# Performance work log

Hardware: AMD Instinct MI355X
Metric: run time of the kernel (lower is better)

The kernel has to match this reference:

```python
import jax, jax.numpy as jnp
import numpy as np

N = 50000      # nodes
E = 800000     # edges (before self loops)
DIN = 128
DOUT = 128
NEG_SLOPE = 0.2  # PyG GATConv default


def setup_inputs() -> dict:
    key = jax.random.key(0)
    k1, k2, k3, k4, k5 = jax.random.split(key, 5)
    x = jax.random.normal(k1, (N, DIN), dtype=jnp.float32)
    edge_index = jax.random.randint(k2, (2, E), 0, N, dtype=jnp.int64)
    # GATConv params (heads=1): lin weight, att_src, att_dst, bias
    W = jax.random.normal(k3, (DIN, DOUT), dtype=jnp.float32) * (1.0 / np.sqrt(DIN))
    att_src = jax.random.normal(k4, (DOUT,), dtype=jnp.float32) * 0.1
    att_dst = jax.random.normal(k5, (DOUT,), dtype=jnp.float32) * 0.1
    bias = jnp.zeros((DOUT,), dtype=jnp.float32)
    return {"x": x, "edge_index": edge_index, "W": W,
            "att_src": att_src, "att_dst": att_dst, "bias": bias}


def reference(x, edge_index, W, att_src, att_dst, bias):
    n = x.shape[0]
    # add_self_loops=True (PyG default)
    loop = jnp.arange(n, dtype=edge_index.dtype)
    src = jnp.concatenate([edge_index[0], loop])  # [E+N] message source
    dst = jnp.concatenate([edge_index[1], loop])  # [E+N] message target

    xw = x @ W                                   # [N, DOUT]
    a_src = xw @ att_src                         # [N] per-node src logit
    a_dst = xw @ att_dst                         # [N] per-node dst logit

    e = jax.nn.leaky_relu(a_src[src] + a_dst[dst], NEG_SLOPE)  # [E+N]
    # segment softmax over destination neighborhoods
    m = jax.ops.segment_max(e, dst, num_segments=n)
    ex = jnp.exp(e - m[dst])
    denom = jax.ops.segment_sum(ex, dst, num_segments=n)
    alpha = ex / denom[dst]                      # [E+N]

    # scatter-aggregate weighted neighbor features
    out = jax.ops.segment_sum(xw[src] * alpha[:, None], dst, num_segments=n)
    out = out + bias
    # outer module applies ELU
    return jax.nn.elu(out)
```

## Files before the change

### kernel.cpp

```cpp
#include <hip/hip_runtime.h>
#include <hip/hip_bf16.h>

#define NNODES 50000
#define NEDGES 800000
#define DIM    128
#define NEG_SLOPE 0.2f

#define MB     64
#define GTILES ((NNODES + MB - 1) / MB)
#define SCHUNK 2346
#define ECHUNK 342
#define FGRID  (GTILES + SCHUNK)
#define CAP    64

#define OFF_XW    0
#define OFF_ASRC  (OFF_XW   + (size_t)NNODES*DIM*2)
#define OFF_ADST  (OFF_ASRC + (size_t)NNODES*4)
#define OFF_CNT   (OFF_ADST + (size_t)NNODES*4)
#define OFF_BKT   (OFF_CNT  + (size_t)(NNODES+16)*4)

typedef __attribute__((ext_vector_type(8))) short bf16x8;
typedef __attribute__((ext_vector_type(4))) float f32x4;

__device__ __forceinline__ float lrelu(float e) {
    return e > 0.f ? e : NEG_SLOPE * e;
}
__device__ __forceinline__ short f2bf(float f) {
    unsigned int u = __float_as_uint(f);
    u += 0x7FFFu + ((u >> 16) & 1u);
    return (short)(u >> 16);
}

__global__ __launch_bounds__(256) void k_front(
    const float* __restrict__ x, const float* __restrict__ W,
    const float* __restrict__ att_src, const float* __restrict__ att_dst,
    const int* __restrict__ ei,
    unsigned short* __restrict__ xwh, float* __restrict__ a_src,
    float* __restrict__ a_dst, int* __restrict__ cnt,
    unsigned short* __restrict__ bucket)
{
    __shared__ short xs[MB * DIM];
    __shared__ short wt[DIM * DIM];
    const int t = threadIdx.x;

    if ((blockIdx.x & 3) != 0) {
        const int sid = blockIdx.x - 1 - (blockIdx.x >> 2);
        const int lo  = sid * ECHUNK;
        int hi = lo + ECHUNK; if (hi > NEDGES) hi = NEDGES;
        for (int e = lo + t; e < hi; e += 256) {
            int src = ei[e], dst = ei[NEDGES + e];
            int pos = atomicAdd(&cnt[dst], 1);
            bucket[(size_t)dst * CAP + (pos & (CAP - 1))] = (unsigned short)src;
        }
        return;
    }

    const int lane = t & 63;
    const int wv   = t >> 6;
    const int c    = lane & 15;
    const int q    = lane >> 4;
    const int base = (blockIdx.x >> 2) * MB;

#pragma unroll
    for (int it = 0; it < 4; ++it) {
        int idx = it * 256 + t;
        int row = idx >> 4, j = idx & 15;
        float4 v0 = {0,0,0,0}, v1 = {0,0,0,0};
        if (base + row < NNODES) {
            const float4* g = (const float4*)(x + (size_t)(base + row) * DIM + j * 8);
            v0 = g[0]; v1 = g[1];
        }
        bf16x8 p;
        p[0]=f2bf(v0.x); p[1]=f2bf(v0.y); p[2]=f2bf(v0.z); p[3]=f2bf(v0.w);
        p[4]=f2bf(v1.x); p[5]=f2bf(v1.y); p[6]=f2bf(v1.z); p[7]=f2bf(v1.w);
        *(bf16x8*)&xs[row * DIM + ((j ^ (row & 15)) * 8)] = p;
    }

    {
        const int n  = t >> 1;
        const int kh = (t & 1) * 64;
#pragma unroll
        for (int jc = 0; jc < 8; ++jc) {
            int kb = kh + jc * 8;
            bf16x8 p;
#pragma unroll
            for (int e = 0; e < 8; ++e)
                p[e] = f2bf(W[(size_t)(kb + e) * DIM + n]);
            int j = kb >> 3;
            *(bf16x8*)&wt[n * DIM + ((j ^ (n & 15)) * 8)] = p;
        }
    }
    __syncthreads();

    f32x4 acc[8];
#pragma unroll
    for (int tt = 0; tt < 8; ++tt) acc[tt] = (f32x4){0.f, 0.f, 0.f, 0.f};

#pragma unroll
    for (int ks = 0; ks < 4; ++ks) {
        int j = ks * 4 + q;
        bf16x8 a = *(const bf16x8*)&xs[(wv * 16 + c) * DIM + ((j ^ c) * 8)];
#pragma unroll
        for (int tt = 0; tt < 8; ++tt) {
            bf16x8 b = *(const bf16x8*)&wt[(tt * 16 + c) * DIM + ((j ^ c) * 8)];
            acc[tt] = __builtin_amdgcn_mfma_f32_16x16x32_bf16(a, b, acc[tt], 0, 0, 0);
        }
    }

    float ps[4] = {0,0,0,0}, pd[4] = {0,0,0,0};
#pragma unroll
    for (int tt = 0; tt < 8; ++tt) {
        float as = att_src[tt * 16 + c];
        float ad = att_dst[tt * 16 + c];
#pragma unroll
        for (int r = 0; r < 4; ++r) {
            ps[r] += as * acc[tt][r];
            pd[r] += ad * acc[tt][r];
        }
    }
#pragma unroll
    for (int off = 1; off < 16; off <<= 1) {
#pragma unroll
        for (int r = 0; r < 4; ++r) {
            ps[r] += __shfl_xor(ps[r], off);
            pd[r] += __shfl_xor(pd[r], off);
        }
    }
    if (c == 0) {
#pragma unroll
        for (int r = 0; r < 4; ++r) {
            int node = base + wv * 16 + q * 4 + r;
            if (node < NNODES) { a_src[node] = ps[r]; a_dst[node] = pd[r]; }
        }
    }

#pragma unroll
    for (int r = 0; r < 4; ++r) {
        int node = base + wv * 16 + q * 4 + r;
        if (node < NNODES) {
#pragma unroll
            for (int tt = 0; tt < 8; ++tt)
                xwh[(size_t)node * DIM + tt * 16 + c] = (unsigned short)f2bf(acc[tt][r]);
        }
    }
}

__global__ __launch_bounds__(256) void k_agg(
    const unsigned short* __restrict__ xwh, const float* __restrict__ a_src,
    const float* __restrict__ a_dst, const int* __restrict__ cnt,
    const unsigned short* __restrict__ bucket, const float* __restrict__ bias,
    float* __restrict__ out)
{
    const int lane = threadIdx.x & 63;
    const int n    = blockIdx.x * 4 + (threadIdx.x >> 6);

    const __hip_bfloat162* __restrict__ xw2 = (const __hip_bfloat162*)xwh;

    const int B = cnt[NNODES];
    int deg = cnt[n] - B;
    deg = deg < CAP ? deg : CAP;
    const int b0 = B & (CAP - 1);

    const float adn = a_dst[n];

    unsigned int src_l = bucket[(size_t)n * CAP + lane];
    if (src_l >= NNODES) src_l = 0;
    float w_l = __expf(lrelu(a_src[src_l] + adn));
    unsigned int u = __float_as_uint(w_l);
    u += 0x7FFFu + ((u >> 16) & 1u);
    const unsigned int entry = (u & 0xFFFF0000u) | src_l;

    float w0 = __expf(lrelu(a_src[n] + adn));
    float2 v0 = __bfloat1622float2(xw2[(size_t)n * 64 + lane]);
    float l = w0;
    float2 acc = { w0 * v0.x, w0 * v0.y };

    for (int j = 0; j < deg; j += 4) {
        float w[4];
        __hip_bfloat162 v[4];
#pragma unroll
        for (int k = 0; k < 4; ++k) {
            if (j + k < deg) {
                unsigned int e = __shfl(entry, (b0 + j + k) & (CAP - 1));
                w[k] = __uint_as_float(e & 0xFFFF0000u);
                v[k] = xw2[(size_t)(e & 0xFFFFu) * 64 + lane];
            } else {
                w[k] = 0.f;
                v[k] = xw2[lane];
            }
        }
#pragma unroll
        for (int k = 0; k < 4; ++k) {
            float2 f = __bfloat1622float2(v[k]);
            acc.x += w[k] * f.x;
            acc.y += w[k] * f.y;
            l += w[k];
        }
    }

    float2 b = ((const float2*)bias)[lane];
    float ox = acc.x / l + b.x;
    float oy = acc.y / l + b.y;
    ox = ox > 0.f ? ox : (__expf(ox) - 1.f);
    oy = oy > 0.f ? oy : (__expf(oy) - 1.f);
    float2 r = { ox, oy };
    ((float2*)out)[(size_t)n * 64 + lane] = r;
}

extern "C" void kernel_launch(void* const* d_in, const int* in_sizes, int n_in,
                              void* d_out, int out_size, void* d_ws, size_t ws_size,
                              hipStream_t stream)
{
    const float* x       = (const float*)d_in[0];
    const int*   ei      = (const int*)d_in[1];
    const float* W       = (const float*)d_in[2];
    const float* att_src = (const float*)d_in[3];
    const float* att_dst = (const float*)d_in[4];
    const float* bias    = (const float*)d_in[5];
    float*       out     = (float*)d_out;

    char* ws = (char*)d_ws;
    unsigned short* xwh = (unsigned short*)(ws + OFF_XW);
    float* a_src  = (float*)(ws + OFF_ASRC);
    float* a_dst  = (float*)(ws + OFF_ADST);
    int*   cnt    = (int*)  (ws + OFF_CNT);
    unsigned short* bucket = (unsigned short*)(ws + OFF_BKT);

    k_front<<<FGRID, 256, 0, stream>>>(x, W, att_src, att_dst, ei,
                                       xwh, a_src, a_dst, cnt, bucket);
    k_agg<<<NNODES / 4, 256, 0, stream>>>(xwh, a_src, a_dst, cnt, bucket, bias, out);
}
```

Measured before the change: 180.3 us.

## Pad degree counters, batch edge scatter, load GEMM A-fragments directly, unroll aggregation

Each degree counter now sits in its own 64-byte slot, which is meant to cut atomic contention and false sharing between neighbouring nodes. The edge-scatter blocks change to one scatter block per GEMM tile, each taking 1024 edges, and issue all loads, then all atomics, then nontemporal bucket stores. The GEMM reads its x A-fragments straight from global into registers and drops the LDS staging buffer for x. The aggregation loop is unrolled to 8 neighbours to keep more gathers in flight, and the output uses nontemporal stores. In exchange the counter array takes much more memory, and the atomics touch more distinct cache lines.

```diff
diff --git a/kernel.cpp b/kernel.cpp
--- a/kernel.cpp
+++ b/kernel.cpp
@@ -8,19 +8,20 @@
 
 #define MB     64
 #define GTILES ((NNODES + MB - 1) / MB)
-#define SCHUNK 2346
-#define ECHUNK 342
-#define FGRID  (GTILES + SCHUNK)
+#define ECHUNK 1024
+#define FGRID  (GTILES * 2)
 #define CAP    64
+#define CSTR   16
 
 #define OFF_XW    0
 #define OFF_ASRC  (OFF_XW   + (size_t)NNODES*DIM*2)
 #define OFF_ADST  (OFF_ASRC + (size_t)NNODES*4)
 #define OFF_CNT   (OFF_ADST + (size_t)NNODES*4)
-#define OFF_BKT   (OFF_CNT  + (size_t)(NNODES+16)*4)
+#define OFF_BKT   (OFF_CNT  + (size_t)(NNODES+1)*CSTR*4)
 
 typedef __attribute__((ext_vector_type(8))) short bf16x8;
 typedef __attribute__((ext_vector_type(4))) float f32x4;
+typedef __attribute__((ext_vector_type(2))) float f32x2;
 
 __device__ __forceinline__ float lrelu(float e) {
     return e > 0.f ? e : NEG_SLOPE * e;
@@ -39,19 +40,29 @@
     float* __restrict__ a_dst, int* __restrict__ cnt,
     unsigned short* __restrict__ bucket)
 {
-    __shared__ short xs[MB * DIM];
     __shared__ short wt[DIM * DIM];
     const int t = threadIdx.x;
 
-    if ((blockIdx.x & 3) != 0) {
-        const int sid = blockIdx.x - 1 - (blockIdx.x >> 2);
+    if (blockIdx.x & 1) {
+        const int sid = blockIdx.x >> 1;
         const int lo  = sid * ECHUNK;
         int hi = lo + ECHUNK; if (hi > NEDGES) hi = NEDGES;
-        for (int e = lo + t; e < hi; e += 256) {
-            int src = ei[e], dst = ei[NEDGES + e];
-            int pos = atomicAdd(&cnt[dst], 1);
-            bucket[(size_t)dst * CAP + (pos & (CAP - 1))] = (unsigned short)src;
-        }
+        int s[4], d[4], p[4];
+#pragma unroll
+        for (int k = 0; k < 4; ++k) {
+            int e = lo + t + (k << 8);
+            if (e < hi) { s[k] = ei[e]; d[k] = ei[NEDGES + e]; }
+            else d[k] = -1;
+        }
+#pragma unroll
+        for (int k = 0; k < 4; ++k)
+            if (d[k] >= 0) p[k] = atomicAdd(&cnt[(size_t)d[k] * CSTR], 1);
+#pragma unroll
+        for (int k = 0; k < 4; ++k)
+            if (d[k] >= 0)
+                __builtin_nontemporal_store(
+                    (unsigned short)s[k],
+                    &bucket[(size_t)d[k] * CAP + (p[k] & (CAP - 1))]);
         return;
     }
 
@@ -59,21 +70,20 @@
     const int wv   = t >> 6;
     const int c    = lane & 15;
     const int q    = lane >> 4;
-    const int base = (blockIdx.x >> 2) * MB;
-
-#pragma unroll
-    for (int it = 0; it < 4; ++it) {
-        int idx = it * 256 + t;
-        int row = idx >> 4, j = idx & 15;
-        float4 v0 = {0,0,0,0}, v1 = {0,0,0,0};
-        if (base + row < NNODES) {
-            const float4* g = (const float4*)(x + (size_t)(base + row) * DIM + j * 8);
-            v0 = g[0]; v1 = g[1];
-        }
-        bf16x8 p;
-        p[0]=f2bf(v0.x); p[1]=f2bf(v0.y); p[2]=f2bf(v0.z); p[3]=f2bf(v0.w);
-        p[4]=f2bf(v1.x); p[5]=f2bf(v1.y); p[6]=f2bf(v1.z); p[7]=f2bf(v1.w);
-        *(bf16x8*)&xs[row * DIM + ((j ^ (row & 15)) * 8)] = p;
+    const int base = (blockIdx.x >> 1) * MB;
+
+    int arow = base + wv * 16 + c;
+    if (arow >= NNODES) arow = 0;
+    const float4* __restrict__ xr = (const float4*)(x + (size_t)arow * DIM);
+    bf16x8 afr[4];
+#pragma unroll
+    for (int ks = 0; ks < 4; ++ks) {
+        int j = ks * 4 + q;
+        float4 v0 = xr[j * 2], v1 = xr[j * 2 + 1];
+        afr[ks][0]=f2bf(v0.x); afr[ks][1]=f2bf(v0.y);
+        afr[ks][2]=f2bf(v0.z); afr[ks][3]=f2bf(v0.w);
+        afr[ks][4]=f2bf(v1.x); afr[ks][5]=f2bf(v1.y);
+        afr[ks][6]=f2bf(v1.z); afr[ks][7]=f2bf(v1.w);
     }
 
     {
@@ -99,11 +109,10 @@
 #pragma unroll
     for (int ks = 0; ks < 4; ++ks) {
         int j = ks * 4 + q;
-        bf16x8 a = *(const bf16x8*)&xs[(wv * 16 + c) * DIM + ((j ^ c) * 8)];
 #pragma unroll
         for (int tt = 0; tt < 8; ++tt) {
             bf16x8 b = *(const bf16x8*)&wt[(tt * 16 + c) * DIM + ((j ^ c) * 8)];
-            acc[tt] = __builtin_amdgcn_mfma_f32_16x16x32_bf16(a, b, acc[tt], 0, 0, 0);
+            acc[tt] = __builtin_amdgcn_mfma_f32_16x16x32_bf16(afr[ks], b, acc[tt], 0, 0, 0);
         }
     }
 
@@ -156,8 +165,8 @@
 
     const __hip_bfloat162* __restrict__ xw2 = (const __hip_bfloat162*)xwh;
 
-    const int B = cnt[NNODES];
-    int deg = cnt[n] - B;
+    const int B = cnt[(size_t)NNODES * CSTR];
+    int deg = cnt[(size_t)n * CSTR] - B;
     deg = deg < CAP ? deg : CAP;
     const int b0 = B & (CAP - 1);
 
@@ -175,11 +184,11 @@
     float l = w0;
     float2 acc = { w0 * v0.x, w0 * v0.y };
 
-    for (int j = 0; j < deg; j += 4) {
-        float w[4];
-        __hip_bfloat162 v[4];
-#pragma unroll
-        for (int k = 0; k < 4; ++k) {
+    for (int j = 0; j < deg; j += 8) {
+        float w[8];
+        __hip_bfloat162 v[8];
+#pragma unroll
+        for (int k = 0; k < 8; ++k) {
             if (j + k < deg) {
                 unsigned int e = __shfl(entry, (b0 + j + k) & (CAP - 1));
                 w[k] = __uint_as_float(e & 0xFFFF0000u);
@@ -190,7 +199,7 @@
             }
         }
 #pragma unroll
-        for (int k = 0; k < 4; ++k) {
+        for (int k = 0; k < 8; ++k) {
             float2 f = __bfloat1622float2(v[k]);
             acc.x += w[k] * f.x;
             acc.y += w[k] * f.y;
@@ -203,8 +212,8 @@
     float oy = acc.y / l + b.y;
     ox = ox > 0.f ? ox : (__expf(ox) - 1.f);
     oy = oy > 0.f ? oy : (__expf(oy) - 1.f);
-    float2 r = { ox, oy };
-    ((float2*)out)[(size_t)n * 64 + lane] = r;
+    f32x2 r = { ox, oy };
+    __builtin_nontemporal_store(r, (f32x2*)out + (size_t)n * 64 + lane);
 }
 
 extern "C" void kernel_launch(void* const* d_in, const int* in_sizes, int n_in,
```

New measurement: 158.6 us. -12.0%, faster.
